# Optimization experiments

Hardware: AMD Instinct MI355X
Metric: run time of the kernel (lower is better)

The kernel has to match this reference:

```python
import jax, jax.numpy as jnp
import numpy as np

NEG_SLOPE = 0.2  # PyG GATConv default


def gat_layer(x, src, dst, W, a_src, a_dst, b, num_nodes):
    """Single-head GATConv (heads=1, add_self_loops handled by caller)."""
    xw = x @ W  # [N, H]
    s_src = xw @ a_src  # [N] per-node source attention logits
    s_dst = xw @ a_dst  # [N]
    e = jax.nn.leaky_relu(s_src[src] + s_dst[dst], NEG_SLOPE)  # [E]
    # segment softmax over incoming edges of each dst node
    m = jax.ops.segment_max(e, dst, num_segments=num_nodes)  # [N]
    ex = jnp.exp(e - m[dst])
    denom = jax.ops.segment_sum(ex, dst, num_segments=num_nodes)  # [N]
    alpha = ex / denom[dst]  # [E]
    out = jax.ops.segment_sum(alpha[:, None] * xw[src], dst, num_segments=num_nodes)
    return out + b


def setup_inputs() -> dict:
    key = jax.random.key(0)
    N, F_IN, H, E, B = 100000, 256, 64, 1000000, 16384
    ks = jax.random.split(key, 16)
    s = lambda fan: 1.0 / np.sqrt(fan)
    return {
        "x": jax.random.normal(ks[0], (N, F_IN), dtype=jnp.float32),
        "edge_index": jax.random.randint(ks[1], (2, E), 0, N, dtype=jnp.int64),
        "user_indices": jax.random.randint(ks[2], (B,), 0, N, dtype=jnp.int64),
        "movie_indices": jax.random.randint(ks[3], (B,), 0, N, dtype=jnp.int64),
        "W1": jax.random.normal(ks[4], (F_IN, H), dtype=jnp.float32) * s(F_IN),
        "a_src1": jax.random.normal(ks[5], (H,), dtype=jnp.float32) * s(H),
        "a_dst1": jax.random.normal(ks[6], (H,), dtype=jnp.float32) * s(H),
        "b1": jnp.zeros((H,), dtype=jnp.float32),
        "W2": jax.random.normal(ks[7], (H, H), dtype=jnp.float32) * s(H),
        "a_src2": jax.random.normal(ks[8], (H,), dtype=jnp.float32) * s(H),
        "a_dst2": jax.random.normal(ks[9], (H,), dtype=jnp.float32) * s(H),
        "b2": jnp.zeros((H,), dtype=jnp.float32),
        "fc_W": jax.random.normal(ks[10], (2 * H, 1), dtype=jnp.float32) * s(2 * H),
        "fc_b": jnp.zeros((1,), dtype=jnp.float32),
    }


def reference(x, edge_index, user_indices, movie_indices,
              W1, a_src1, a_dst1, b1, W2, a_src2, a_dst2, b2, fc_W, fc_b):
    N = x.shape[0]
    # PyG GATConv default add_self_loops=True: append (i, i) edges
    loops = jnp.arange(N, dtype=edge_index.dtype)
    src = jnp.concatenate([edge_index[0], loops])
    dst = jnp.concatenate([edge_index[1], loops])
    h = gat_layer(x, src, dst, W1, a_src1, a_dst1, b1, N)
    h = jax.nn.relu(h)
    h = gat_layer(h, src, dst, W2, a_src2, a_dst2, b2, N)
    combined = jnp.concatenate([h[user_indices], h[movie_indices]], axis=1)  # [B, 2H]
    return combined @ fc_W + fc_b  # [B, 1]
```

## Files before the change

kernel.cpp:

```cpp
#include <hip/hip_runtime.h>
#include <hip/hip_bf16.h>
#include <hip/hip_fp16.h>

#define LRELU_SLOPE 0.2f
#define CSR_STRIDE 32

__device__ __forceinline__ float lrelu(float x) { return x > 0.f ? x : LRELU_SLOPE * x; }

typedef __attribute__((ext_vector_type(8))) short short8;
typedef __attribute__((ext_vector_type(4))) float f32x4;

__device__ __forceinline__ unsigned short f2bf(float f) {
    unsigned u = __builtin_bit_cast(unsigned, f);
    u = (u + 0x7FFFu + ((u >> 16) & 1u)) >> 16;
    return (unsigned short)u;
}
__device__ __forceinline__ float bf2f(unsigned short b) {
    unsigned u = ((unsigned)b) << 16;
    return __builtin_bit_cast(float, u);
}

template <int K>
__device__ __forceinline__ void packW_body(const float* __restrict__ W,
                                           unsigned short* __restrict__ Bhi,
                                           unsigned short* __restrict__ Blo,
                                           int blk, int t) {
    constexpr int NKC = K / 32;
    int g = blk * 256 + t;
    if (g >= 4 * NKC * 64) return;
    int lane = g & 63;
    int kc = (g >> 6) % NKC;
    int ct = g / (64 * NKC);
    int qd = lane >> 4, col = lane & 15;
    #pragma unroll
    for (int j = 0; j < 8; j++) {
        int k = kc * 32 + qd * 8 + j;
        float w = W[(size_t)k * 64 + ct * 16 + col];
        unsigned short h = f2bf(w);
        float rem = w - bf2f(h);
        Bhi[(size_t)g * 8 + j] = h;
        Blo[(size_t)g * 8 + j] = f2bf(rem);
    }
}

__global__ __launch_bounds__(256) void k_prep(const float* __restrict__ W1,
                                              unsigned short* __restrict__ b1hi, unsigned short* __restrict__ b1lo,
                                              const float* __restrict__ W2,
                                              unsigned short* __restrict__ b2hi, unsigned short* __restrict__ b2lo,
                                              int* __restrict__ deg, int* __restrict__ ovfCnt, int N) {
    int b = blockIdx.x;
    if (b < 8)  { packW_body<256>(W1, b1hi, b1lo, b, threadIdx.x); return; }
    if (b < 10) { packW_body<64>(W2, b2hi, b2lo, b - 8, threadIdx.x); return; }
    int i = (b - 10) * 256 + threadIdx.x;
    if (i < N) deg[i] = 0;
    if (i == 0) *ovfCnt = 0;
}

__global__ void k_build(const int* __restrict__ src, const int* __restrict__ dst,
                        int* __restrict__ deg, int* __restrict__ csr,
                        int* __restrict__ ovfCnt, int2* __restrict__ ovf, int E) {
    int i = (blockIdx.x * blockDim.x + threadIdx.x) * 4;
    if (i + 3 < E) {
        int4 d4 = *(const int4*)(dst + i);
        int4 s4 = *(const int4*)(src + i);
        int p0 = atomicAdd(&deg[d4.x], 1);
        int p1 = atomicAdd(&deg[d4.y], 1);
        int p2 = atomicAdd(&deg[d4.z], 1);
        int p3 = atomicAdd(&deg[d4.w], 1);
        if (p0 < CSR_STRIDE) csr[d4.x * CSR_STRIDE + p0] = s4.x;
        else { int o = atomicAdd(ovfCnt, 1); ovf[o] = make_int2(d4.x, s4.x); }
        if (p1 < CSR_STRIDE) csr[d4.y * CSR_STRIDE + p1] = s4.y;
        else { int o = atomicAdd(ovfCnt, 1); ovf[o] = make_int2(d4.y, s4.y); }
        if (p2 < CSR_STRIDE) csr[d4.z * CSR_STRIDE + p2] = s4.z;
        else { int o = atomicAdd(ovfCnt, 1); ovf[o] = make_int2(d4.z, s4.z); }
        if (p3 < CSR_STRIDE) csr[d4.w * CSR_STRIDE + p3] = s4.w;
        else { int o = atomicAdd(ovfCnt, 1); ovf[o] = make_int2(d4.w, s4.w); }
    } else {
        for (int j = i; j < E; j++) {
            int d = dst[j], s = src[j];
            int p = atomicAdd(&deg[d], 1);
            if (p < CSR_STRIDE) csr[d * CSR_STRIDE + p] = s;
            else { int o = atomicAdd(ovfCnt, 1); ovf[o] = make_int2(d, s); }
        }
    }
}

template <int K>
__device__ __forceinline__ void mfma_body(const float* __restrict__ X,
                                          const unsigned short* __restrict__ Bhi,
                                          const unsigned short* __restrict__ Blo,
                                          const float* __restrict__ a_s, const float* __restrict__ a_d,
                                          __half* __restrict__ XW, float* __restrict__ Ssrc,
                                          float* __restrict__ Sdst, int N, int blk) {
    constexpr int NKC = K / 32;
    int t = threadIdx.x, lane = t & 63, wid = t >> 6;
    int mtile = blk * 4 + wid;
    if (mtile * 16 >= N) return;
    int m0 = mtile * 16;
    int qd = lane >> 4, col = lane & 15;

    int rA = m0 + col;
    rA = rA < N ? rA : N - 1;
    const float* xrow = X + (size_t)rA * K + qd * 8;

    const short8* bh = (const short8*)Bhi;
    const short8* bl = (const short8*)Blo;

    f32x4 acc[4];
    #pragma unroll
    for (int ct = 0; ct < 4; ct++) acc[ct] = (f32x4){0.f, 0.f, 0.f, 0.f};

    #pragma clang loop unroll(disable)
    for (int kc = 0; kc < NKC; kc++) {
        const float* xp = xrow + kc * 32;
        float4 xa = *(const float4*)xp;
        float4 xb = *(const float4*)(xp + 4);
        float xv[8] = {xa.x, xa.y, xa.z, xa.w, xb.x, xb.y, xb.z, xb.w};
        short8 ah, al;
        #pragma unroll
        for (int j = 0; j < 8; j++) {
            unsigned short h = f2bf(xv[j]);
            ah[j] = (short)h;
            al[j] = (short)f2bf(xv[j] - bf2f(h));
        }
        #pragma unroll
        for (int ct = 0; ct < 4; ct++) {
            short8 wh = bh[(ct * NKC + kc) * 64 + lane];
            short8 wl = bl[(ct * NKC + kc) * 64 + lane];
            acc[ct] = __builtin_amdgcn_mfma_f32_16x16x32_bf16(ah, wh, acc[ct], 0, 0, 0);
            acc[ct] = __builtin_amdgcn_mfma_f32_16x16x32_bf16(al, wh, acc[ct], 0, 0, 0);
            acc[ct] = __builtin_amdgcn_mfma_f32_16x16x32_bf16(ah, wl, acc[ct], 0, 0, 0);
        }
    }

    float asx[4], adx[4];
    #pragma unroll
    for (int ct = 0; ct < 4; ct++) {
        asx[ct] = a_s[ct * 16 + col];
        adx[ct] = a_d[ct * 16 + col];
    }
    #pragma unroll
    for (int r = 0; r < 4; r++) {
        int row = m0 + qd * 4 + r;
        if (row < N) {
            float vs = 0.f, vd = 0.f;
            #pragma unroll
            for (int ct = 0; ct < 4; ct++) {
                float v = acc[ct][r];
                XW[(size_t)row * 64 + ct * 16 + col] = __float2half(v);
                vs += v * asx[ct];
                vd += v * adx[ct];
            }
            #pragma unroll
            for (int d = 1; d < 16; d <<= 1) {
                vs += __shfl_xor(vs, d);
                vd += __shfl_xor(vd, d);
            }
            if (col == 0) { Ssrc[row] = vs; Sdst[row] = vd; }
        }
    }
}

template <int K>
__global__ __launch_bounds__(256) void k_mfma(const float* __restrict__ X,
                                              const unsigned short* __restrict__ Bhi,
                                              const unsigned short* __restrict__ Blo,
                                              const float* __restrict__ a_s, const float* __restrict__ a_d,
                                              __half* __restrict__ XW, float* __restrict__ Ssrc,
                                              float* __restrict__ Sdst, int N) {
    mfma_body<K>(X, Bhi, Blo, a_s, a_d, XW, Ssrc, Sdst, N, blockIdx.x);
}

__global__ __launch_bounds__(256) void k_attn(const __half* __restrict__ XW, const float* __restrict__ Ssrc,
                                              const float* __restrict__ Sdst, const int* __restrict__ csr,
                                              const int* __restrict__ deg,
                                              const int* __restrict__ ovfCnt, const int2* __restrict__ ovf,
                                              const int* __restrict__ uiL, const int* __restrict__ miL, int Bn,
                                              const float* __restrict__ bias, float* __restrict__ H,
                                              int N, int do_relu) {
    int t = threadIdx.x, lane = t & 63, wid = t >> 6;
    int q = lane >> 4;
    int c = lane & 15;
    int i4 = (blockIdx.x * 4 + wid) * 4 + q;
    bool valid;
    int n;
    if (uiL) {
        valid = i4 < 2 * Bn;
        n = valid ? (i4 < Bn ? uiL[i4] : miL[i4 - Bn]) : 0;
    } else {
        valid = i4 < N;
        n = valid ? i4 : 0;
    }
    int nc = n;

    int d = deg[nc];
    int st = nc * CSR_STRIDE;
    float sd = Sdst[nc];
    int d32 = d < CSR_STRIDE ? d : CSR_STRIDE;
    int dcap = d < 16 ? d : 16;

    int myS = 0;
    if (c < dcap) myS = csr[st + c];

    int s0 = __shfl(myS, q * 16 + 0), s1 = __shfl(myS, q * 16 + 1);
    int s2 = __shfl(myS, q * 16 + 2), s3 = __shfl(myS, q * 16 + 3);
    float2 rs = *(const float2*)(XW + (size_t)nc * 64 + c * 4);
    float2 r0 = *(const float2*)(XW + (size_t)s0 * 64 + c * 4);
    float2 r1 = *(const float2*)(XW + (size_t)s1 * 64 + c * 4);
    float2 r2 = *(const float2*)(XW + (size_t)s2 * 64 + c * 4);
    float2 r3 = *(const float2*)(XW + (size_t)s3 * 64 + c * 4);

    float wself = __expf(lrelu(Ssrc[nc] + sd));
    float myW = 0.f;
    if (c < dcap) myW = __expf(lrelu(Ssrc[myS] + sd));
    float dpart = myW + ((c == 0) ? wself : 0.f);

    float4 acc4 = make_float4(0.f, 0.f, 0.f, 0.f);
    auto accum = [&](float2 raw, float w) {
        const __half2* hp = (const __half2*)&raw;
        float2 f0 = __half22float2(hp[0]);
        float2 f1 = __half22float2(hp[1]);
        acc4.x += w * f0.x; acc4.y += w * f0.y; acc4.z += w * f1.x; acc4.w += w * f1.y;
    };

    float w0 = __shfl(myW, q * 16 + 0), w1 = __shfl(myW, q * 16 + 1);
    float w2 = __shfl(myW, q * 16 + 2), w3 = __shfl(myW, q * 16 + 3);
    accum(rs, wself);
    accum(r0, w0); accum(r1, w1); accum(r2, w2); accum(r3, w3);

    for (int i = 4; i < dcap; i += 4) {
        int t0 = __shfl(myS, q * 16 + i + 0), t1 = __shfl(myS, q * 16 + i + 1);
        int t2 = __shfl(myS, q * 16 + i + 2), t3 = __shfl(myS, q * 16 + i + 3);
        float2 q0 = *(const float2*)(XW + (size_t)t0 * 64 + c * 4);
        float2 q1 = *(const float2*)(XW + (size_t)t1 * 64 + c * 4);
        float2 q2 = *(const float2*)(XW + (size_t)t2 * 64 + c * 4);
        float2 q3 = *(const float2*)(XW + (size_t)t3 * 64 + c * 4);
        float v0 = __shfl(myW, q * 16 + i + 0), v1 = __shfl(myW, q * 16 + i + 1);
        float v2 = __shfl(myW, q * 16 + i + 2), v3 = __shfl(myW, q * 16 + i + 3);
        accum(q0, v0); accum(q1, v1); accum(q2, v2); accum(q3, v3);
    }

    for (int i = 16; i < d32; i++) {
        int s = csr[st + i];
        float w = __expf(lrelu(Ssrc[s] + sd));
        if (c == 0) dpart += w;
        float2 qv = *(const float2*)(XW + (size_t)s * 64 + c * 4);
        accum(qv, w);
    }

    int nov = *ovfCnt;
    if (nov > 0) {
        for (int j = 0; j < nov; j++) {
            int2 e = ovf[j];
            if (e.x == nc) {
                float w = __expf(lrelu(Ssrc[e.y] + sd));
                if (c == 0) dpart += w;
                float2 qv = *(const float2*)(XW + (size_t)e.y * 64 + c * 4);
                accum(qv, w);
            }
        }
    }

    #pragma unroll
    for (int dd = 8; dd > 0; dd >>= 1) dpart += __shfl_xor(dpart, dd);

    if (valid) {
        float4 b4 = *(const float4*)&bias[c * 4];
        float inv = 1.f / dpart;
        float4 o;
        o.x = acc4.x * inv + b4.x;
        o.y = acc4.y * inv + b4.y;
        o.z = acc4.z * inv + b4.z;
        o.w = acc4.w * inv + b4.w;
        if (do_relu) {
            o.x = fmaxf(o.x, 0.f); o.y = fmaxf(o.y, 0.f);
            o.z = fmaxf(o.z, 0.f); o.w = fmaxf(o.w, 0.f);
        }
        *(float4*)&H[(size_t)n * 64 + c * 4] = o;
    }
}

__global__ __launch_bounds__(256) void k_head(const float* __restrict__ H, const int* __restrict__ ui,
                                              const int* __restrict__ mi, const float* __restrict__ fcW,
                                              const float* __restrict__ fcb, float* __restrict__ out, int B) {
    int t = threadIdx.x, lane = t & 63, wid = t >> 6;
    int i = blockIdx.x * 4 + wid;
    if (i >= B) return;
    int u = ui[i], m = mi[i];
    float v = H[(size_t)u * 64 + lane] * fcW[lane] + H[(size_t)m * 64 + lane] * fcW[64 + lane];
    #pragma unroll
    for (int dd = 32; dd > 0; dd >>= 1) v += __shfl_xor(v, dd);
    if (lane == 0) out[i] = v + fcb[0];
}

extern "C" void kernel_launch(void* const* d_in, const int* in_sizes, int n_in,
                              void* d_out, int out_size, void* d_ws, size_t ws_size,
                              hipStream_t stream) {
    const float* x   = (const float*)d_in[0];
    const int*   ei  = (const int*)d_in[1];
    const int*   ui  = (const int*)d_in[2];
    const int*   mi  = (const int*)d_in[3];
    const float* W1  = (const float*)d_in[4];
    const float* as1 = (const float*)d_in[5];
    const float* ad1 = (const float*)d_in[6];
    const float* b1  = (const float*)d_in[7];
    const float* W2  = (const float*)d_in[8];
    const float* as2 = (const float*)d_in[9];
    const float* ad2 = (const float*)d_in[10];
    const float* b2  = (const float*)d_in[11];
    const float* fcW = (const float*)d_in[12];
    const float* fcb = (const float*)d_in[13];
    float* out = (float*)d_out;

    const int Hdim = in_sizes[5];
    const int FIN  = in_sizes[4] / Hdim;
    const int N    = in_sizes[0] / FIN;
    const int E    = in_sizes[1] / 2;
    const int B    = in_sizes[2];

    char* w = (char*)d_ws;
    auto alloc = [&](size_t bytes) -> void* {
        void* p = (void*)w;
        w += (bytes + 255) & ~(size_t)255;
        return p;
    };
    __half* xw  = (__half*)alloc((size_t)N * 64 * 2);
    float* hbuf = (float*)alloc((size_t)N * 64 * 4);
    float* ssrc = (float*)alloc((size_t)N * 4);
    float* sdst = (float*)alloc((size_t)N * 4);
    int* deg    = (int*)alloc((size_t)N * 4);
    int* csr    = (int*)alloc((size_t)N * CSR_STRIDE * 4);
    int* ovfCnt = (int*)alloc(256);
    int2* ovf   = (int2*)alloc((size_t)65536 * 8);
    unsigned short* b1hi = (unsigned short*)alloc((size_t)4 * 8 * 64 * 8 * 2);
    unsigned short* b1lo = (unsigned short*)alloc((size_t)4 * 8 * 64 * 8 * 2);
    unsigned short* b2hi = (unsigned short*)alloc((size_t)4 * 2 * 64 * 8 * 2);
    unsigned short* b2lo = (unsigned short*)alloc((size_t)4 * 2 * 64 * 8 * 2);

    const int* esrc = ei;
    const int* edst = ei + E;

    const int mfmaBlocks = ((N + 15) / 16 + 3) / 4;
    const int attnBlocks = (N + 15) / 16;
    const int attn2Blocks = (2 * B + 15) / 16;

    int prepBlocks = 10 + (N + 255) / 256;
    k_prep<<<prepBlocks, 256, 0, stream>>>(W1, b1hi, b1lo, W2, b2hi, b2lo, deg, ovfCnt, N);

    k_build<<<(E / 4 + 255) / 256, 256, 0, stream>>>(esrc, edst, deg, csr, ovfCnt, ovf, E);

    k_mfma<256><<<mfmaBlocks, 256, 0, stream>>>(x, b1hi, b1lo, as1, ad1, xw, ssrc, sdst, N);
    k_attn<<<attnBlocks, 256, 0, stream>>>(xw, ssrc, sdst, csr, deg, ovfCnt, ovf,
                                           (const int*)nullptr, (const int*)nullptr, 0, b1, hbuf, N, 1);

    k_mfma<64><<<mfmaBlocks, 256, 0, stream>>>(hbuf, b2hi, b2lo, as2, ad2, xw, ssrc, sdst, N);
    k_attn<<<attn2Blocks, 256, 0, stream>>>(xw, ssrc, sdst, csr, deg, ovfCnt, ovf,
                                            ui, mi, B, b2, hbuf, N, 0);

    k_head<<<(B + 3) / 4, 256, 0, stream>>>(hbuf, ui, mi, fcW, fcb, out, B);
}
```

Before: 332.4 us.

## Inline degree into CSR row header and fuse FC head into layer-2 attention

The per-node degree counter moves into slot 0 of each CSR row, so the degree load shares a cache line with the neighbor list. This drops the separate deg array and leaves 31 inline slots per row, with more edges spilling to overflow. The final linear head is fused into the second attention kernel: each user or movie half computes its dot with fcW and atomically adds it into out, which k_prep pre-initializes with the bias. This removes one kernel launch and the hbuf round trip, at the cost of float atomics and non-deterministic summation order.

```diff
diff --git a/kernel.cpp b/kernel.cpp
--- a/kernel.cpp
+++ b/kernel.cpp
@@ -47,39 +47,42 @@
                                               unsigned short* __restrict__ b1hi, unsigned short* __restrict__ b1lo,
                                               const float* __restrict__ W2,
                                               unsigned short* __restrict__ b2hi, unsigned short* __restrict__ b2lo,
-                                              int* __restrict__ deg, int* __restrict__ ovfCnt, int N) {
+                                              int* __restrict__ csr, int* __restrict__ ovfCnt,
+                                              float* __restrict__ out, const float* __restrict__ fcb,
+                                              int N, int B) {
     int b = blockIdx.x;
     if (b < 8)  { packW_body<256>(W1, b1hi, b1lo, b, threadIdx.x); return; }
     if (b < 10) { packW_body<64>(W2, b2hi, b2lo, b - 8, threadIdx.x); return; }
     int i = (b - 10) * 256 + threadIdx.x;
-    if (i < N) deg[i] = 0;
+    if (i < N) csr[(size_t)i * CSR_STRIDE] = 0;
+    if (i < B) out[i] = fcb[0];
     if (i == 0) *ovfCnt = 0;
 }
 
 __global__ void k_build(const int* __restrict__ src, const int* __restrict__ dst,
-                        int* __restrict__ deg, int* __restrict__ csr,
+                        int* __restrict__ csr,
                         int* __restrict__ ovfCnt, int2* __restrict__ ovf, int E) {
     int i = (blockIdx.x * blockDim.x + threadIdx.x) * 4;
     if (i + 3 < E) {
         int4 d4 = *(const int4*)(dst + i);
         int4 s4 = *(const int4*)(src + i);
-        int p0 = atomicAdd(&deg[d4.x], 1);
-        int p1 = atomicAdd(&deg[d4.y], 1);
-        int p2 = atomicAdd(&deg[d4.z], 1);
-        int p3 = atomicAdd(&deg[d4.w], 1);
-        if (p0 < CSR_STRIDE) csr[d4.x * CSR_STRIDE + p0] = s4.x;
+        int p0 = atomicAdd(&csr[(size_t)d4.x * CSR_STRIDE], 1);
+        int p1 = atomicAdd(&csr[(size_t)d4.y * CSR_STRIDE], 1);
+        int p2 = atomicAdd(&csr[(size_t)d4.z * CSR_STRIDE], 1);
+        int p3 = atomicAdd(&csr[(size_t)d4.w * CSR_STRIDE], 1);
+        if (p0 < CSR_STRIDE - 1) csr[(size_t)d4.x * CSR_STRIDE + 1 + p0] = s4.x;
         else { int o = atomicAdd(ovfCnt, 1); ovf[o] = make_int2(d4.x, s4.x); }
-        if (p1 < CSR_STRIDE) csr[d4.y * CSR_STRIDE + p1] = s4.y;
+        if (p1 < CSR_STRIDE - 1) csr[(size_t)d4.y * CSR_STRIDE + 1 + p1] = s4.y;
         else { int o = atomicAdd(ovfCnt, 1); ovf[o] = make_int2(d4.y, s4.y); }
-        if (p2 < CSR_STRIDE) csr[d4.z * CSR_STRIDE + p2] = s4.z;
+        if (p2 < CSR_STRIDE - 1) csr[(size_t)d4.z * CSR_STRIDE + 1 + p2] = s4.z;
         else { int o = atomicAdd(ovfCnt, 1); ovf[o] = make_int2(d4.z, s4.z); }
-        if (p3 < CSR_STRIDE) csr[d4.w * CSR_STRIDE + p3] = s4.w;
+        if (p3 < CSR_STRIDE - 1) csr[(size_t)d4.w * CSR_STRIDE + 1 + p3] = s4.w;
         else { int o = atomicAdd(ovfCnt, 1); ovf[o] = make_int2(d4.w, s4.w); }
     } else {
         for (int j = i; j < E; j++) {
             int d = dst[j], s = src[j];
-            int p = atomicAdd(&deg[d], 1);
-            if (p < CSR_STRIDE) csr[d * CSR_STRIDE + p] = s;
+            int p = atomicAdd(&csr[(size_t)d * CSR_STRIDE], 1);
+            if (p < CSR_STRIDE - 1) csr[(size_t)d * CSR_STRIDE + 1 + p] = s;
             else { int o = atomicAdd(ovfCnt, 1); ovf[o] = make_int2(d, s); }
         }
     }
@@ -173,10 +176,10 @@
 
 __global__ __launch_bounds__(256) void k_attn(const __half* __restrict__ XW, const float* __restrict__ Ssrc,
                                               const float* __restrict__ Sdst, const int* __restrict__ csr,
-                                              const int* __restrict__ deg,
                                               const int* __restrict__ ovfCnt, const int2* __restrict__ ovf,
                                               const int* __restrict__ uiL, const int* __restrict__ miL, int Bn,
                                               const float* __restrict__ bias, float* __restrict__ H,
+                                              const float* __restrict__ fcW, float* __restrict__ out,
                                               int N, int do_relu) {
     int t = threadIdx.x, lane = t & 63, wid = t >> 6;
     int q = lane >> 4;
@@ -193,14 +196,14 @@
     }
     int nc = n;
 
-    int d = deg[nc];
     int st = nc * CSR_STRIDE;
+    int d = csr[st];
     float sd = Sdst[nc];
-    int d32 = d < CSR_STRIDE ? d : CSR_STRIDE;
+    int d31 = d < CSR_STRIDE - 1 ? d : CSR_STRIDE - 1;
     int dcap = d < 16 ? d : 16;
 
     int myS = 0;
-    if (c < dcap) myS = csr[st + c];
+    if (c < dcap) myS = csr[st + 1 + c];
 
     int s0 = __shfl(myS, q * 16 + 0), s1 = __shfl(myS, q * 16 + 1);
     int s2 = __shfl(myS, q * 16 + 2), s3 = __shfl(myS, q * 16 + 3);
@@ -240,8 +243,8 @@
         accum(q0, v0); accum(q1, v1); accum(q2, v2); accum(q3, v3);
     }
 
-    for (int i = 16; i < d32; i++) {
-        int s = csr[st + i];
+    for (int i = 16; i < d31; i++) {
+        int s = csr[st + 1 + i];
         float w = __expf(lrelu(Ssrc[s] + sd));
         if (c == 0) dpart += w;
         float2 qv = *(const float2*)(XW + (size_t)s * 64 + c * 4);
@@ -276,21 +279,16 @@
             o.x = fmaxf(o.x, 0.f); o.y = fmaxf(o.y, 0.f);
             o.z = fmaxf(o.z, 0.f); o.w = fmaxf(o.w, 0.f);
         }
-        *(float4*)&H[(size_t)n * 64 + c * 4] = o;
-    }
-}
-
-__global__ __launch_bounds__(256) void k_head(const float* __restrict__ H, const int* __restrict__ ui,
-                                              const int* __restrict__ mi, const float* __restrict__ fcW,
-                                              const float* __restrict__ fcb, float* __restrict__ out, int B) {
-    int t = threadIdx.x, lane = t & 63, wid = t >> 6;
-    int i = blockIdx.x * 4 + wid;
-    if (i >= B) return;
-    int u = ui[i], m = mi[i];
-    float v = H[(size_t)u * 64 + lane] * fcW[lane] + H[(size_t)m * 64 + lane] * fcW[64 + lane];
-    #pragma unroll
-    for (int dd = 32; dd > 0; dd >>= 1) v += __shfl_xor(v, dd);
-    if (lane == 0) out[i] = v + fcb[0];
+        if (!uiL) {
+            *(float4*)&H[(size_t)n * 64 + c * 4] = o;
+        } else {
+            const float* fw = fcW + (i4 < Bn ? 0 : 64) + c * 4;
+            float dot = o.x * fw[0] + o.y * fw[1] + o.z * fw[2] + o.w * fw[3];
+            #pragma unroll
+            for (int dd = 8; dd > 0; dd >>= 1) dot += __shfl_xor(dot, dd);
+            if (c == 0) atomicAdd(&out[i4 < Bn ? i4 : i4 - Bn], dot);
+        }
+    }
 }
 
 extern "C" void kernel_launch(void* const* d_in, const int* in_sizes, int n_in,
@@ -328,7 +326,6 @@
     float* hbuf = (float*)alloc((size_t)N * 64 * 4);
     float* ssrc = (float*)alloc((size_t)N * 4);
     float* sdst = (float*)alloc((size_t)N * 4);
-    int* deg    = (int*)alloc((size_t)N * 4);
     int* csr    = (int*)alloc((size_t)N * CSR_STRIDE * 4);
     int* ovfCnt = (int*)alloc(256);
     int2* ovf   = (int2*)alloc((size_t)65536 * 8);
@@ -345,17 +342,16 @@
     const int attn2Blocks = (2 * B + 15) / 16;
 
     int prepBlocks = 10 + (N + 255) / 256;
-    k_prep<<<prepBlocks, 256, 0, stream>>>(W1, b1hi, b1lo, W2, b2hi, b2lo, deg, ovfCnt, N);
-
-    k_build<<<(E / 4 + 255) / 256, 256, 0, stream>>>(esrc, edst, deg, csr, ovfCnt, ovf, E);
+    k_prep<<<prepBlocks, 256, 0, stream>>>(W1, b1hi, b1lo, W2, b2hi, b2lo, csr, ovfCnt, out, fcb, N, B);
+
+    k_build<<<(E / 4 + 255) / 256, 256, 0, stream>>>(esrc, edst, csr, ovfCnt, ovf, E);
 
     k_mfma<256><<<mfmaBlocks, 256, 0, stream>>>(x, b1hi, b1lo, as1, ad1, xw, ssrc, sdst, N);
-    k_attn<<<attnBlocks, 256, 0, stream>>>(xw, ssrc, sdst, csr, deg, ovfCnt, ovf,
-                                           (const int*)nullptr, (const int*)nullptr, 0, b1, hbuf, N, 1);
+    k_attn<<<attnBlocks, 256, 0, stream>>>(xw, ssrc, sdst, csr, ovfCnt, ovf,
+                                           (const int*)nullptr, (const int*)nullptr, 0,
+                                           b1, hbuf, (const float*)nullptr, (float*)nullptr, N, 1);
 
     k_mfma<64><<<mfmaBlocks, 256, 0, stream>>>(hbuf, b2hi, b2lo, as2, ad2, xw, ssrc, sdst, N);
-    k_attn<<<attn2Blocks, 256, 0, stream>>>(xw, ssrc, sdst, csr, deg, ovfCnt, ovf,
-                                            ui, mi, B, b2, hbuf, N, 0);
-
-    k_head<<<(B + 3) / 4, 256, 0, stream>>>(hbuf, ui, mi, fcW, fcb, out, B);
-}
+    k_attn<<<attn2Blocks, 256, 0, stream>>>(xw, ssrc, sdst, csr, ovfCnt, ovf,
+                                            ui, mi, B, b2, hbuf, fcW, out, N, 0);
+}
```

Measured after the change: 303.5 us. 8.7% less time.
